# Optimization experiments

Hardware: AMD Instinct MI355X
Metric: run time of the kernel (lower is better)

Reference implementation:

```python
import jax, jax.numpy as jnp
import numpy as np

NUM_ITERS = 3

def squash(s, axis=-1):
    # standard capsule squash: ||s||^2/(1+||s||^2) * s/||s||
    sq = jnp.sum(s * s, axis=axis, keepdims=True)
    norm = jnp.sqrt(sq)
    return (sq / (1.0 + sq)) * (s / norm)

def setup_inputs() -> dict:
    key = jax.random.key(0)
    kx, kw = jax.random.split(key)
    B, I, k, l, O = 512, 1152, 8, 16, 7
    x = jax.random.normal(kx, (B, I, k), dtype=jnp.float32)
    w = jax.random.normal(kw, (I, k, l, O), dtype=jnp.float32)
    return {"x": x, "w": w}

def reference(x, w):
    # x: [B, I, k]; w: [I, k, l, O]
    u_hat = jnp.einsum('BIk,IklO->BIlO', x, w)            # [B, I, l, O]
    I, _, l, _ = w.shape
    b_ij = jnp.zeros((I, l), dtype=u_hat.dtype)
    v_j = None
    for _ in range(NUM_ITERS):
        c_ij = jax.nn.softmax(b_ij, axis=0)               # softmax over I
        s_j = jnp.einsum('Il,BIlO->BlO', c_ij, u_hat)     # [B, l, O]
        v_j = jnp.transpose(squash(s_j), (0, 2, 1))       # [B, O, l]
        u_vj = jnp.einsum('BOl,BIlO->BIl', v_j, u_hat).mean(axis=0)  # [I, l]
        b_ij = b_ij + u_vj
    return v_j
```

## Files before the change

### kernel.cpp

```cpp
#include <hip/hip_runtime.h>
#include <hip/hip_bf16.h>


#define NB 512
#define NI 1152
#define NLO 112
#define NIK 9216
#define KSPLIT 96
#define SPART 57344

typedef __attribute__((ext_vector_type(8))) short bf16x8;
typedef __attribute__((ext_vector_type(4))) float f32x4;

__device__ __forceinline__ ushort f2bf(float f) {
    __hip_bfloat16 h = __float2bfloat16(f);
    return *(ushort*)&h;
}

__device__ __forceinline__ void conv_x_body(const float* __restrict__ x,
                                            ushort* __restrict__ xbf,
                                            ushort* __restrict__ xT, int bid) {
    __shared__ ushort tile[64][68];
    int kg = bid % 144, bg = bid / 144;
    int k0 = kg * 64, b0 = bg * 64;
    int t = threadIdx.x;
    for (int e = t; e < 1024; e += 256) {
        int r = e >> 4, c4 = (e & 15) * 4;
        float4 f = *(const float4*)&x[(size_t)(b0 + r) * NIK + k0 + c4];
        ushort4 u = { f2bf(f.x), f2bf(f.y), f2bf(f.z), f2bf(f.w) };
        *(ushort4*)&xbf[(size_t)(b0 + r) * NIK + k0 + c4] = u;
        tile[r][c4] = u.x; tile[r][c4 + 1] = u.y; tile[r][c4 + 2] = u.z; tile[r][c4 + 3] = u.w;
    }
    __syncthreads();
    for (int e = t; e < 1024; e += 256) {
        int kr = e >> 4, c4 = (e & 15) * 4;
        ushort4 u = { tile[c4][kr], tile[c4 + 1][kr], tile[c4 + 2][kr], tile[c4 + 3][kr] };
        *(ushort4*)&xT[(size_t)(k0 + kr) * NB + b0 + c4] = u;
    }
}

__global__ __launch_bounds__(256) void prep0(const float* __restrict__ x,
                                             ushort* __restrict__ xbf,
                                             ushort* __restrict__ xT,
                                             const float* __restrict__ w,
                                             ushort* __restrict__ wcT,
                                             float* __restrict__ Z) {
    if (blockIdx.x < 1152) { conv_x_body(x, xbf, xT, blockIdx.x); return; }
    __shared__ ushort tile[NLO][66];
    int t = threadIdx.x;
    int ik0 = (blockIdx.x - 1152) * 64;
    if (blockIdx.x == 1152 && t < 48) Z[t] = (t < 16) ? 1.0f : 0.0f;
    const float cv = 1.0f / 1152.0f;
    for (int e = t; e < 7168; e += 256) {
        int ikl = e / NLO, lo = e - ikl * NLO;
        tile[lo][ikl] = f2bf(cv * w[(size_t)(ik0 + ikl) * NLO + lo]);
    }
    __syncthreads();
    for (int e = t; e < 7168; e += 256) {
        int lo = e >> 6, ikl = e & 63;
        wcT[(size_t)lo * NIK + ik0 + ikl] = tile[lo][ikl];
    }
}

__global__ __launch_bounds__(256) void s_gemm(const ushort* __restrict__ xbf,
                                              const ushort* __restrict__ wcT,
                                              float* __restrict__ part) {
    int wid = blockIdx.x * 4 + (threadIdx.x >> 6);
    int lane = threadIdx.x & 63;
    int mt = wid & 31;
    int kc = wid >> 5;
    int b0 = mt * 16, k0 = kc * 96;
    int row = lane & 15, quad = lane >> 4;
    const ushort* ap = xbf + (size_t)(b0 + row) * NIK + k0 + quad * 8;
    const ushort* bp = wcT + (size_t)row * NIK + k0 + quad * 8;
    f32x4 acc[7];
    #pragma unroll
    for (int nt = 0; nt < 7; ++nt) acc[nt] = (f32x4){0.f, 0.f, 0.f, 0.f};
    #pragma unroll
    for (int ks = 0; ks < 3; ++ks) {
        bf16x8 a = *(const bf16x8*)(ap + ks * 32);
        #pragma unroll
        for (int nt = 0; nt < 7; ++nt) {
            bf16x8 bfr = *(const bf16x8*)(bp + (size_t)nt * 16 * NIK + ks * 32);
            acc[nt] = __builtin_amdgcn_mfma_f32_16x16x32_bf16(a, bfr, acc[nt], 0, 0, 0);
        }
    }
    float* pp = part + (size_t)kc * SPART + (size_t)(b0 + quad * 4) * NLO + row;
    #pragma unroll
    for (int nt = 0; nt < 7; ++nt)
        #pragma unroll
        for (int r = 0; r < 4; ++r)
            pp[(size_t)r * NLO + nt * 16] = acc[nt][r];
}

__global__ void squash_k(const float* __restrict__ part, ushort* __restrict__ vT,
                         float* __restrict__ out, const float* __restrict__ Zit,
                         int write_out) {
    int b = blockIdx.x;
    int t = threadIdx.x;
    __shared__ float sh[NLO];
    __shared__ float fac[16];
    __shared__ float zinv[16];
    if (t >= 112 && t < 128) zinv[t - 112] = 1.0f / Zit[t - 112];
    float sv = 0.f;
    if (t < NLO) {
        const float* p = part + (size_t)b * NLO + t;
        #pragma unroll 8
        for (int kc = 0; kc < KSPLIT; ++kc) sv += p[(size_t)kc * SPART];
    }
    __syncthreads();
    if (t < NLO) { sv *= zinv[t / 7]; sh[t] = sv; }
    __syncthreads();
    if (t < 16) {
        float sq = 0.f;
        #pragma unroll
        for (int o = 0; o < 7; ++o) { float e = sh[t * 7 + o]; sq += e * e; }
        fac[t] = sqrtf(sq) / (1.0f + sq);
    }
    __syncthreads();
    if (t < NLO) {
        int l = t / 7, o = t - l * 7;
        float vv = sv * fac[l];
        vT[(size_t)(o * 16 + l) * NB + b] = f2bf(vv);
        if (write_out) out[(size_t)b * NLO + o * 16 + l] = vv;
    }
}

__global__ __launch_bounds__(512) void g_wc(const ushort* __restrict__ xT,
                                            const ushort* __restrict__ vT,
                                            const float* __restrict__ w,
                                            float* __restrict__ bij,
                                            ushort* __restrict__ wcT,
                                            float* __restrict__ Zit, int accum) {
    __shared__ float bs[2][8][16];
    __shared__ float cs[128];
    __shared__ ushort tile[NLO][66];
    int t = threadIdx.x;
    int wv = t >> 6;
    int lane = t & 63;
    int half = wv & 1;
    int mt = wv >> 1;
    int m0 = blockIdx.x * 64 + mt * 16;
    int kb0 = half * 256;
    int row = lane & 15, quad = lane >> 4;
    const ushort* ap = xT + (size_t)(m0 + row) * NB + kb0 + quad * 8;
    const ushort* bp = vT + (size_t)row * NB + kb0 + quad * 8;
    f32x4 acc[7];
    #pragma unroll
    for (int nt = 0; nt < 7; ++nt) acc[nt] = (f32x4){0.f, 0.f, 0.f, 0.f};
    #pragma unroll
    for (int ks = 0; ks < 8; ++ks) {
        bf16x8 a = *(const bf16x8*)(ap + ks * 32);
        #pragma unroll
        for (int nt = 0; nt < 7; ++nt) {
            bf16x8 bfr = *(const bf16x8*)(bp + (size_t)nt * 16 * NB + ks * 32);
            acc[nt] = __builtin_amdgcn_mfma_f32_16x16x32_bf16(a, bfr, acc[nt], 0, 0, 0);
        }
    }
    float S = 0.f;
    #pragma unroll
    for (int r = 0; r < 4; ++r) {
        int ik = m0 + quad * 4 + r;
        const float* wr = w + (size_t)ik * NLO + row * 7;
        float p = 0.f;
        #pragma unroll
        for (int o = 0; o < 7; ++o) p += wr[o] * acc[o][r];
        S += p;
    }
    float Sp = __shfl_down(S, 16);
    if ((quad & 1) == 0)
        bs[half][mt * 2 + (quad >> 1)][row] = (S + Sp) * (1.0f / 512.0f);
    __syncthreads();
    if (t < 128) {
        int il = t >> 4, l = t & 15;
        int i = blockIdx.x * 8 + il;
        float val = bs[0][il][l] + bs[1][il][l];
        if (accum) val += bij[i * 16 + l];
        bij[i * 16 + l] = val;
        cs[t] = expf(val);
    }
    __syncthreads();
    if (t < 16) {
        float z = 0.f;
        #pragma unroll
        for (int j = 0; j < 8; ++j) z += cs[j * 16 + t];
        atomicAdd(&Zit[t], z);
    }
    int ik0 = blockIdx.x * 64;
    for (int e = t; e < 7168; e += 512) {
        int ikl = e / NLO, lo = e - ikl * NLO;
        int il = ((ikl >> 3) << 4) + lo / 7;
        tile[lo][ikl] = f2bf(cs[il] * w[(size_t)(ik0 + ikl) * NLO + lo]);
    }
    __syncthreads();
    for (int e = t; e < 7168; e += 512) {
        int lo = e >> 6, ikl = e & 63;
        wcT[(size_t)lo * NIK + ik0 + ikl] = tile[lo][ikl];
    }
}

extern "C" void kernel_launch(void* const* d_in, const int* in_sizes, int n_in,
                              void* d_out, int out_size, void* d_ws, size_t ws_size,
                              hipStream_t stream) {
    const float* x = (const float*)d_in[0];
    const float* w = (const float*)d_in[1];
    float* out = (float*)d_out;
    float* ws = (float*)d_ws;
    float*  f_bij  = ws;
    float*  f_Z    = f_bij + NI * 16;
    float*  f_part = f_Z + 48;
    ushort* xbf    = (ushort*)(f_part + (size_t)KSPLIT * SPART);
    ushort* xT     = xbf + (size_t)NB * NIK;
    ushort* wcT    = xT + (size_t)NIK * NB;
    ushort* vT     = wcT + (size_t)NLO * NIK;
    prep0<<<1296, 256, 0, stream>>>(x, xbf, xT, w, wcT, f_Z);
    for (int it = 0; it < 3; ++it) {
        s_gemm<<<768, 256, 0, stream>>>(xbf, wcT, f_part);
        squash_k<<<512, 128, 0, stream>>>(f_part, vT, out, f_Z + it * 16,
                                          it == 2 ? 1 : 0);
        if (it < 2)
            g_wc<<<144, 512, 0, stream>>>(xT, vT, w, f_bij, wcT,
                                          f_Z + (it + 1) * 16, it);
    }
}
```

Before: 177.4 us.

## Fuse s-GEMM split-K reduction and squash into one padded-N kernel

Replaces the split-K s_gemm, which wrote 96 fp32 partial slabs to global memory, and the separate squash kernel with one kernel. In it, 16 waves per block split K and reduce through shared memory, then apply the softmax normalization and squash in place. The weight matrix is padded from 112 to 128 columns (o padded 7->8) so each block owns two whole capsules and can compute the squash norm locally. This removes the partial-buffer round trip and one launch per iteration. In exchange it adds some wasted MFMA work on padded columns and has only 256 blocks, each doing a longer serial K loop per wave.

New measurement: 178.4 us. Within noise of the previous version (+0.5%).

```diff
diff --git a/kernel.cpp b/kernel.cpp
--- a/kernel.cpp
+++ b/kernel.cpp
@@ -6,8 +6,7 @@
 #define NI 1152
 #define NLO 112
 #define NIK 9216
-#define KSPLIT 96
-#define SPART 57344
+#define NPAD 128
 
 typedef __attribute__((ext_vector_type(8))) short bf16x8;
 typedef __attribute__((ext_vector_type(4))) float f32x4;
@@ -43,86 +42,80 @@
                                              ushort* __restrict__ xbf,
                                              ushort* __restrict__ xT,
                                              const float* __restrict__ w,
-                                             ushort* __restrict__ wcT,
+                                             ushort* __restrict__ wcTp,
                                              float* __restrict__ Z) {
     if (blockIdx.x < 1152) { conv_x_body(x, xbf, xT, blockIdx.x); return; }
-    __shared__ ushort tile[NLO][66];
+    __shared__ ushort tile[NPAD][66];
     int t = threadIdx.x;
     int ik0 = (blockIdx.x - 1152) * 64;
     if (blockIdx.x == 1152 && t < 48) Z[t] = (t < 16) ? 1.0f : 0.0f;
     const float cv = 1.0f / 1152.0f;
-    for (int e = t; e < 7168; e += 256) {
-        int ikl = e / NLO, lo = e - ikl * NLO;
-        tile[lo][ikl] = f2bf(cv * w[(size_t)(ik0 + ikl) * NLO + lo]);
-    }
-    __syncthreads();
-    for (int e = t; e < 7168; e += 256) {
-        int lo = e >> 6, ikl = e & 63;
-        wcT[(size_t)lo * NIK + ik0 + ikl] = tile[lo][ikl];
-    }
-}
-
-__global__ __launch_bounds__(256) void s_gemm(const ushort* __restrict__ xbf,
-                                              const ushort* __restrict__ wcT,
-                                              float* __restrict__ part) {
-    int wid = blockIdx.x * 4 + (threadIdx.x >> 6);
-    int lane = threadIdx.x & 63;
-    int mt = wid & 31;
-    int kc = wid >> 5;
-    int b0 = mt * 16, k0 = kc * 96;
+    for (int e = t; e < 8192; e += 256) {
+        int ikl = e >> 7, np = e & 127;
+        int l = np >> 3, o = np & 7;
+        float wv = (o < 7) ? w[(size_t)(ik0 + ikl) * NLO + l * 7 + o] : 0.f;
+        tile[np][ikl] = f2bf(cv * wv);
+    }
+    __syncthreads();
+    for (int e = t; e < 8192; e += 256) {
+        int np = e >> 6, ikl = e & 63;
+        wcTp[(size_t)np * NIK + ik0 + ikl] = tile[np][ikl];
+    }
+}
+
+__global__ __launch_bounds__(1024) void sq_gemm(const ushort* __restrict__ xbf,
+                                                const ushort* __restrict__ wcTp,
+                                                const float* __restrict__ Zit,
+                                                ushort* __restrict__ vT,
+                                                float* __restrict__ out, int wout) {
+    __shared__ float sp[16][16][16];
+    __shared__ float ss[16][16];
+    __shared__ float facs[16][2];
+    __shared__ float zi[2];
+    int bid = blockIdx.x;
+    int mt = bid & 31, ng = bid >> 5;
+    int b0 = mt * 16, n0 = ng * 16;
+    int t = threadIdx.x;
+    int wv = t >> 6, lane = t & 63;
     int row = lane & 15, quad = lane >> 4;
+    int k0 = wv * 576;
     const ushort* ap = xbf + (size_t)(b0 + row) * NIK + k0 + quad * 8;
-    const ushort* bp = wcT + (size_t)row * NIK + k0 + quad * 8;
-    f32x4 acc[7];
-    #pragma unroll
-    for (int nt = 0; nt < 7; ++nt) acc[nt] = (f32x4){0.f, 0.f, 0.f, 0.f};
-    #pragma unroll
-    for (int ks = 0; ks < 3; ++ks) {
+    const ushort* bp = wcTp + (size_t)(n0 + row) * NIK + k0 + quad * 8;
+    f32x4 acc = {0.f, 0.f, 0.f, 0.f};
+    #pragma unroll 6
+    for (int ks = 0; ks < 18; ++ks) {
         bf16x8 a = *(const bf16x8*)(ap + ks * 32);
-        #pragma unroll
-        for (int nt = 0; nt < 7; ++nt) {
-            bf16x8 bfr = *(const bf16x8*)(bp + (size_t)nt * 16 * NIK + ks * 32);
-            acc[nt] = __builtin_amdgcn_mfma_f32_16x16x32_bf16(a, bfr, acc[nt], 0, 0, 0);
+        bf16x8 b = *(const bf16x8*)(bp + ks * 32);
+        acc = __builtin_amdgcn_mfma_f32_16x16x32_bf16(a, b, acc, 0, 0, 0);
+    }
+    if (t < 2) zi[t] = 1.0f / Zit[ng * 2 + t];
+    #pragma unroll
+    for (int r = 0; r < 4; ++r) sp[wv][quad * 4 + r][row] = acc[r];
+    __syncthreads();
+    if (t < 256) {
+        int m = t >> 4, n = t & 15;
+        float sv = 0.f;
+        #pragma unroll
+        for (int w8 = 0; w8 < 16; ++w8) sv += sp[w8][m][n];
+        ss[m][n] = sv * zi[n >> 3];
+    }
+    __syncthreads();
+    if (t < 32) {
+        int m = t >> 1, ll = t & 1;
+        float sq = 0.f;
+        #pragma unroll
+        for (int o = 0; o < 8; ++o) { float e = ss[m][ll * 8 + o]; sq += e * e; }
+        facs[m][ll] = sqrtf(sq) / (1.0f + sq);
+    }
+    __syncthreads();
+    if (t < 256) {
+        int m = t >> 4, n = t & 15;
+        int o = n & 7, lg = ng * 2 + (n >> 3);
+        if (o < 7) {
+            float vv = ss[m][n] * facs[m][n >> 3];
+            vT[(size_t)(o * 16 + lg) * NB + b0 + m] = f2bf(vv);
+            if (wout) out[(size_t)(b0 + m) * NLO + o * 16 + lg] = vv;
         }
-    }
-    float* pp = part + (size_t)kc * SPART + (size_t)(b0 + quad * 4) * NLO + row;
-    #pragma unroll
-    for (int nt = 0; nt < 7; ++nt)
-        #pragma unroll
-        for (int r = 0; r < 4; ++r)
-            pp[(size_t)r * NLO + nt * 16] = acc[nt][r];
-}
-
-__global__ void squash_k(const float* __restrict__ part, ushort* __restrict__ vT,
-                         float* __restrict__ out, const float* __restrict__ Zit,
-                         int write_out) {
-    int b = blockIdx.x;
-    int t = threadIdx.x;
-    __shared__ float sh[NLO];
-    __shared__ float fac[16];
-    __shared__ float zinv[16];
-    if (t >= 112 && t < 128) zinv[t - 112] = 1.0f / Zit[t - 112];
-    float sv = 0.f;
-    if (t < NLO) {
-        const float* p = part + (size_t)b * NLO + t;
-        #pragma unroll 8
-        for (int kc = 0; kc < KSPLIT; ++kc) sv += p[(size_t)kc * SPART];
-    }
-    __syncthreads();
-    if (t < NLO) { sv *= zinv[t / 7]; sh[t] = sv; }
-    __syncthreads();
-    if (t < 16) {
-        float sq = 0.f;
-        #pragma unroll
-        for (int o = 0; o < 7; ++o) { float e = sh[t * 7 + o]; sq += e * e; }
-        fac[t] = sqrtf(sq) / (1.0f + sq);
-    }
-    __syncthreads();
-    if (t < NLO) {
-        int l = t / 7, o = t - l * 7;
-        float vv = sv * fac[l];
-        vT[(size_t)(o * 16 + l) * NB + b] = f2bf(vv);
-        if (write_out) out[(size_t)b * NLO + o * 16 + l] = vv;
     }
 }
 
@@ -130,11 +123,11 @@
                                             const ushort* __restrict__ vT,
                                             const float* __restrict__ w,
                                             float* __restrict__ bij,
-                                            ushort* __restrict__ wcT,
+                                            ushort* __restrict__ wcTp,
                                             float* __restrict__ Zit, int accum) {
     __shared__ float bs[2][8][16];
     __shared__ float cs[128];
-    __shared__ ushort tile[NLO][66];
+    __shared__ ushort tile[NPAD][66];
     int t = threadIdx.x;
     int wv = t >> 6;
     int lane = t & 63;
@@ -187,15 +180,17 @@
         atomicAdd(&Zit[t], z);
     }
     int ik0 = blockIdx.x * 64;
-    for (int e = t; e < 7168; e += 512) {
-        int ikl = e / NLO, lo = e - ikl * NLO;
-        int il = ((ikl >> 3) << 4) + lo / 7;
-        tile[lo][ikl] = f2bf(cs[il] * w[(size_t)(ik0 + ikl) * NLO + lo]);
-    }
-    __syncthreads();
-    for (int e = t; e < 7168; e += 512) {
-        int lo = e >> 6, ikl = e & 63;
-        wcT[(size_t)lo * NIK + ik0 + ikl] = tile[lo][ikl];
+    for (int e = t; e < 8192; e += 512) {
+        int ikl = e >> 7, np = e & 127;
+        int l = np >> 3, o = np & 7;
+        int il = ((ikl >> 3) << 4) + l;
+        float wv_ = (o < 7) ? w[(size_t)(ik0 + ikl) * NLO + l * 7 + o] : 0.f;
+        tile[np][ikl] = f2bf(cs[il] * wv_);
+    }
+    __syncthreads();
+    for (int e = t; e < 8192; e += 512) {
+        int np = e >> 6, ikl = e & 63;
+        wcTp[(size_t)np * NIK + ik0 + ikl] = tile[np][ikl];
     }
 }
 
@@ -208,18 +203,16 @@
     float* ws = (float*)d_ws;
     float*  f_bij  = ws;
     float*  f_Z    = f_bij + NI * 16;
-    float*  f_part = f_Z + 48;
-    ushort* xbf    = (ushort*)(f_part + (size_t)KSPLIT * SPART);
+    ushort* xbf    = (ushort*)(f_Z + 48);
     ushort* xT     = xbf + (size_t)NB * NIK;
-    ushort* wcT    = xT + (size_t)NIK * NB;
-    ushort* vT     = wcT + (size_t)NLO * NIK;
-    prep0<<<1296, 256, 0, stream>>>(x, xbf, xT, w, wcT, f_Z);
+    ushort* wcTp   = xT + (size_t)NIK * NB;
+    ushort* vT     = wcTp + (size_t)NPAD * NIK;
+    prep0<<<1296, 256, 0, stream>>>(x, xbf, xT, w, wcTp, f_Z);
     for (int it = 0; it < 3; ++it) {
-        s_gemm<<<768, 256, 0, stream>>>(xbf, wcT, f_part);
-        squash_k<<<512, 128, 0, stream>>>(f_part, vT, out, f_Z + it * 16,
+        sq_gemm<<<256, 1024, 0, stream>>>(xbf, wcTp, f_Z + it * 16, vT, out,
                                           it == 2 ? 1 : 0);
         if (it < 2)
-            g_wc<<<144, 512, 0, stream>>>(xT, vT, w, f_bij, wcT,
+            g_wc<<<144, 512, 0, stream>>>(xT, vT, w, f_bij, wcTp,
                                           f_Z + (it + 1) * 16, it);
     }
 }
```
